# Kernel tuning notes

Measured on AMD Instinct MI355X. Metric: run time of the kernel, lower is better.

The kernel has to match this reference:

```python
import jax, jax.numpy as jnp
import numpy as np

N_ROWS = 262144
FEAT = 1024
N_CORES = 4096
SEG = N_ROWS // N_CORES
H1 = H2 = H3 = 1024
NUM_CLASSES = 2
BN_EPS = 1e-5


def setup_inputs() -> dict:
    key = jax.random.key(0)
    ks = jax.random.split(key, 12)
    x = jax.random.normal(ks[0], (N_ROWS, FEAT), dtype=jnp.float32)
    # equal-length segments: start indices 0, SEG, 2*SEG, ...
    corelen = (jnp.arange(N_CORES) * SEG).astype(jnp.int64)
    def lin(k, din, dout):
        kw, kb = jax.random.split(k)
        W = jax.random.normal(kw, (din, dout), dtype=jnp.float32) / np.sqrt(din)
        b = jnp.zeros((dout,), dtype=jnp.float32)
        return W, b
    W1, b1 = lin(ks[1], FEAT, H1)
    W2, b2 = lin(ks[2], H1, H2)
    W3, b3 = lin(ks[3], H2, H3)
    W4, b4 = lin(ks[4], H3, NUM_CLASSES)
    g1 = jnp.ones((H1,), jnp.float32); be1 = jnp.zeros((H1,), jnp.float32)
    g2 = jnp.ones((H2,), jnp.float32); be2 = jnp.zeros((H2,), jnp.float32)
    g3 = jnp.ones((H3,), jnp.float32); be3 = jnp.zeros((H3,), jnp.float32)
    return {"x": x, "corelen": corelen,
            "W1": W1, "b1": b1, "g1": g1, "be1": be1,
            "W2": W2, "b2": b2, "g2": g2, "be2": be2,
            "W3": W3, "b3": b3, "g3": g3, "be3": be3,
            "W4": W4, "b4": b4}


def _batchnorm(h, g, b):
    # BatchNorm1d, training mode: biased batch statistics over the batch dim
    m = jnp.mean(h, axis=0)
    v = jnp.mean(jnp.square(h - m), axis=0)
    return g * (h - m) * jax.lax.rsqrt(v + BN_EPS) + b


def reference(x, corelen, W1, b1, g1, be1, W2, b2, g2, be2, W3, b3, g3, be3, W4, b4):
    n = x.shape[0]
    # segment id of row r = number of starts <= r, minus 1 (rows before
    # corelen[0] get id -1 and are dropped, matching the torch loop)
    seg_ids = jnp.searchsorted(corelen, jnp.arange(n), side="right") - 1
    agg = jax.ops.segment_sum(x, seg_ids, num_segments=corelen.shape[0])  # [C, FEAT]
    h = jax.nn.relu(_batchnorm(agg @ W1 + b1, g1, be1))
    h = jax.nn.relu(_batchnorm(h @ W2 + b2, g2, be2))
    h = jax.nn.relu(_batchnorm(h @ W3 + b3, g3, be3))
    return h @ W4 + b4  # [C, NUM_CLASSES]
```

## Files before the change

kernel.cpp:

```cpp
#include <hip/hip_runtime.h>
#include <hip/hip_bf16.h>
#include <stdint.h>

#define N_ROWS 262144
#define FEAT 1024
#define N_CORES 4096
#define HDIM 1024
#define BN_EPS 1e-5f

typedef __attribute__((ext_vector_type(8))) short bf16x8;
typedef __attribute__((ext_vector_type(4))) float f32x4;

__device__ __forceinline__ unsigned short f2bf(float f) {
  __hip_bfloat16 h = __float2bfloat16(f);
  return __builtin_bit_cast(unsigned short, h);
}
__device__ __forceinline__ float bf2f(unsigned short u) {
  unsigned int x = ((unsigned int)u) << 16;
  return __builtin_bit_cast(float, x);
}

__device__ __forceinline__ void gll16(const unsigned short* g, unsigned short* l) {
  __builtin_amdgcn_global_load_lds(
      (const __attribute__((address_space(1))) void*)g,
      (__attribute__((address_space(3))) void*)l, 16, 0, 0);
}

__global__ __launch_bounds__(256)
void k_segsum(const float* __restrict__ x, const int* __restrict__ corelen,
              unsigned short* __restrict__ aggb) {
  const int seg = blockIdx.x;
  const int t = threadIdx.x;
  const int start = corelen[seg];
  const int end = (seg + 1 < N_CORES) ? corelen[seg + 1] : N_ROWS;
  float4 a0 = make_float4(0.f, 0.f, 0.f, 0.f);
  float4 a1 = make_float4(0.f, 0.f, 0.f, 0.f);
  const float* xp = x + (size_t)start * FEAT + t * 4;
  int r = start;
  for (; r + 2 <= end; r += 2) {
    const float4 v0 = *(const float4*)xp;
    const float4 v1 = *(const float4*)(xp + FEAT);
    a0.x += v0.x; a0.y += v0.y; a0.z += v0.z; a0.w += v0.w;
    a1.x += v1.x; a1.y += v1.y; a1.z += v1.z; a1.w += v1.w;
    xp += 2 * FEAT;
  }
  if (r < end) {
    const float4 v0 = *(const float4*)xp;
    a0.x += v0.x; a0.y += v0.y; a0.z += v0.z; a0.w += v0.w;
  }
  a0.x += a1.x; a0.y += a1.y; a0.z += a1.z; a0.w += a1.w;
  ushort4 o;
  o.x = f2bf(a0.x); o.y = f2bf(a0.y); o.z = f2bf(a0.z); o.w = f2bf(a0.w);
  *(ushort4*)(aggb + (size_t)seg * FEAT + t * 4) = o;
}

__global__ __launch_bounds__(256)
void k_transpose_bf16(const float* __restrict__ W, unsigned short* __restrict__ Wt) {
  __shared__ unsigned short tile[32][33];
  const int tx = threadIdx.x, ty = threadIdx.y;
  const int n0 = blockIdx.x * 32, k0 = blockIdx.y * 32;
#pragma unroll
  for (int i = 0; i < 4; ++i)
    tile[ty + 8 * i][tx] = f2bf(W[(size_t)(k0 + ty + 8 * i) * HDIM + n0 + tx]);
  __syncthreads();
#pragma unroll
  for (int i = 0; i < 4; ++i)
    Wt[(size_t)(n0 + ty + 8 * i) * HDIM + k0 + tx] = tile[tx][ty + 8 * i];
}

#define BM 128
#define BN 64
#define BK 64
__global__ __launch_bounds__(256)
void k_gemm_bt(const unsigned short* __restrict__ A,
               const unsigned short* __restrict__ Bt,
               const float* __restrict__ bias,
               float* __restrict__ C,
               float* __restrict__ sums, float* __restrict__ sumsq) {
  __shared__ unsigned short As[BM * BK];
  __shared__ unsigned short Bs[BN * BK];
  const int t = threadIdx.x;
  const int lane = t & 63;
  const int w = t >> 6;
  const int tileM = blockIdx.x * BM;
  const int tileN = blockIdx.y * BN;
  const int wr = (w >> 1) * 64;
  const int wc = (w & 1) * 32;
  const int fr = lane & 15;
  const int kk = (lane >> 4) * 8;
  const int lr = lane >> 3;
  const int sc = ((lane & 7) * 8) ^ (lr << 3);

  const unsigned short* pA = A + (size_t)(tileM + w * 32 + lr) * HDIM + sc;
  const unsigned short* pB = Bt + (size_t)(tileN + w * 16 + lr) * HDIM + sc;

  f32x4 acc[4][2] = {};

  for (int k0 = 0; k0 < HDIM; k0 += BK) {
#pragma unroll
    for (int j = 0; j < 4; ++j)
      gll16(pA + k0 + j * 8 * HDIM, As + (w * 32 + j * 8) * BK);
#pragma unroll
    for (int j = 0; j < 2; ++j)
      gll16(pB + k0 + j * 8 * HDIM, Bs + (w * 16 + j * 8) * BK);
    __syncthreads();
#pragma unroll
    for (int ks = 0; ks < 2; ++ks) {
      const int pc = (ks * 32 + kk) ^ ((fr & 7) << 3);
      bf16x8 af[4], bf[2];
#pragma unroll
      for (int m = 0; m < 4; ++m)
        af[m] = *(const bf16x8*)&As[(wr + m * 16 + fr) * BK + pc];
#pragma unroll
      for (int n = 0; n < 2; ++n)
        bf[n] = *(const bf16x8*)&Bs[(wc + n * 16 + fr) * BK + pc];
#pragma unroll
      for (int m = 0; m < 4; ++m)
#pragma unroll
        for (int n = 0; n < 2; ++n)
          acc[m][n] = __builtin_amdgcn_mfma_f32_16x16x32_bf16(af[m], bf[n], acc[m][n], 0, 0, 0);
    }
    __syncthreads();
  }

  const int cr = (lane >> 4) * 4;
  const int cc = lane & 15;
#pragma unroll
  for (int n = 0; n < 2; ++n) {
    const int col = tileN + wc + n * 16 + cc;
    const float bv = bias[col];
    float s = 0.f, s2 = 0.f;
#pragma unroll
    for (int m = 0; m < 4; ++m) {
      float* cp = C + (size_t)(tileM + wr + m * 16 + cr) * HDIM + col;
#pragma unroll
      for (int j = 0; j < 4; ++j) {
        const float h = acc[m][n][j] + bv;
        cp[(size_t)j * HDIM] = h;
        s += h; s2 += h * h;
      }
    }
    s  += __shfl_xor(s, 16, 64);  s  += __shfl_xor(s, 32, 64);
    s2 += __shfl_xor(s2, 16, 64); s2 += __shfl_xor(s2, 32, 64);
    if ((lane >> 4) == 0) {
      atomicAdd(&sums[col], s);
      atomicAdd(&sumsq[col], s2);
    }
  }
}

__global__ __launch_bounds__(256)
void k_finalize(const float* __restrict__ sums, const float* __restrict__ sumsq,
                const float* __restrict__ g, const float* __restrict__ be,
                float* __restrict__ scale, float* __restrict__ shift) {
  const int c = blockIdx.x * 256 + threadIdx.x;
  const float mean = sums[c] * (1.f / N_CORES);
  const float var = sumsq[c] * (1.f / N_CORES) - mean * mean;
  const float sc = g[c] * rsqrtf(var + BN_EPS);
  scale[c] = sc;
  shift[c] = be[c] - mean * sc;
}

__global__ __launch_bounds__(256)
void k_norm_relu(const float* __restrict__ Hp, const float* __restrict__ scale,
                 const float* __restrict__ shift, unsigned short* __restrict__ Ab) {
  const size_t i4 = ((size_t)blockIdx.x * 256 + threadIdx.x) * 4;
  const float4 v = *(const float4*)(Hp + i4);
  const int c = (int)(i4 & (HDIM - 1));
  const float4 sc = *(const float4*)(scale + c);
  const float4 sh = *(const float4*)(shift + c);
  ushort4 o;
  o.x = f2bf(fmaxf(v.x * sc.x + sh.x, 0.f));
  o.y = f2bf(fmaxf(v.y * sc.y + sh.y, 0.f));
  o.z = f2bf(fmaxf(v.z * sc.z + sh.z, 0.f));
  o.w = f2bf(fmaxf(v.w * sc.w + sh.w, 0.f));
  *(ushort4*)(Ab + i4) = o;
}

__global__ __launch_bounds__(256)
void k_final(const unsigned short* __restrict__ Ab, const float* __restrict__ W4,
             const float* __restrict__ b4, float* __restrict__ out) {
  const int t = threadIdx.x;
  const int w = t >> 6, lane = t & 63;
  const int row = blockIdx.x * 4 + w;
  const unsigned short* a = Ab + (size_t)row * HDIM + lane * 16;
  const bf16x8 v0 = *(const bf16x8*)a;
  const bf16x8 v1 = *(const bf16x8*)(a + 8);
  float s0 = 0.f, s1 = 0.f;
  const int kbase = lane * 16;
#pragma unroll
  for (int j = 0; j < 8; ++j) {
    const float av = bf2f((unsigned short)v0[j]);
    s0 += av * W4[(kbase + j) * 2 + 0];
    s1 += av * W4[(kbase + j) * 2 + 1];
  }
#pragma unroll
  for (int j = 0; j < 8; ++j) {
    const float av = bf2f((unsigned short)v1[j]);
    s0 += av * W4[(kbase + 8 + j) * 2 + 0];
    s1 += av * W4[(kbase + 8 + j) * 2 + 1];
  }
#pragma unroll
  for (int off = 32; off >= 1; off >>= 1) {
    s0 += __shfl_down(s0, off, 64);
    s1 += __shfl_down(s1, off, 64);
  }
  if (lane == 0) {
    out[row * 2 + 0] = s0 + b4[0];
    out[row * 2 + 1] = s1 + b4[1];
  }
}

extern "C" void kernel_launch(void* const* d_in, const int* in_sizes, int n_in,
                              void* d_out, int out_size, void* d_ws, size_t ws_size,
                              hipStream_t stream) {
  (void)in_sizes; (void)n_in; (void)out_size; (void)ws_size;
  const float* x       = (const float*)d_in[0];
  const int* corelen   = (const int*)d_in[1];
  const float* W1  = (const float*)d_in[2];
  const float* b1  = (const float*)d_in[3];
  const float* g1  = (const float*)d_in[4];
  const float* be1 = (const float*)d_in[5];
  const float* W2  = (const float*)d_in[6];
  const float* b2  = (const float*)d_in[7];
  const float* g2  = (const float*)d_in[8];
  const float* be2 = (const float*)d_in[9];
  const float* W3  = (const float*)d_in[10];
  const float* b3  = (const float*)d_in[11];
  const float* g3  = (const float*)d_in[12];
  const float* be3 = (const float*)d_in[13];
  const float* W4  = (const float*)d_in[14];
  const float* b4  = (const float*)d_in[15];
  float* out = (float*)d_out;

  char* ws = (char*)d_ws;
  float* Hpre          = (float*)(ws);
  unsigned short* Abf  = (unsigned short*)(ws + (16u << 20));
  unsigned short* Wt   = (unsigned short*)(ws + (24u << 20));
  float* stats = (float*)(ws + (26u << 20));
  float* scale = stats + 6 * HDIM;
  float* shift = scale + HDIM;

  hipMemsetAsync(stats, 0, 6 * HDIM * sizeof(float), stream);
  k_segsum<<<N_CORES, 256, 0, stream>>>(x, corelen, Abf);

  const float* Ws[3]  = {W1, W2, W3};
  const float* bs[3]  = {b1, b2, b3};
  const float* gs[3]  = {g1, g2, g3};
  const float* bes[3] = {be1, be2, be3};
  for (int l = 0; l < 3; ++l) {
    float* sums  = stats + l * 2 * HDIM;
    float* sumsq = sums + HDIM;
    k_transpose_bf16<<<dim3(32, 32), dim3(32, 8), 0, stream>>>(Ws[l], Wt);
    k_gemm_bt<<<dim3(N_CORES / BM, HDIM / BN), 256, 0, stream>>>(
        Abf, Wt, bs[l], Hpre, sums, sumsq);
    k_finalize<<<HDIM / 256, 256, 0, stream>>>(sums, sumsq, gs[l], bes[l], scale, shift);
    k_norm_relu<<<(N_CORES * HDIM / 4) / 256, 256, 0, stream>>>(Hpre, scale, shift, Abf);
  }
  k_final<<<N_CORES / 4, 256, 0, stream>>>(Abf, W4, b4, out);
}
```

Baseline: 300.7 us.

## Double-buffer GEMM LDS, store bf16 pre-activations, batch weight transposes

Adds double-buffered LDS staging in the GEMM so the next K tile's global-to-LDS loads are issued before computing the current one, and remaps block indices for cache locality. Pre-BatchNorm activations are stored as bf16 instead of fp32, halving traffic between GEMM and norm kernels, and the norm kernel processes 8 elements per thread. All three weight transposes run in one launch ahead of the layer loop. Storing pre-activations in bf16 adds rounding before normalization, and double buffering doubles LDS use, which may reduce occupancy.

```diff
diff --git a/kernel.cpp b/kernel.cpp
--- a/kernel.cpp
+++ b/kernel.cpp
@@ -9,6 +9,7 @@
 #define BN_EPS 1e-5f
 
 typedef __attribute__((ext_vector_type(8))) short bf16x8;
+typedef __attribute__((ext_vector_type(8))) unsigned short u16x8;
 typedef __attribute__((ext_vector_type(4))) float f32x4;
 
 __device__ __forceinline__ unsigned short f2bf(float f) {
@@ -55,8 +56,12 @@
 }
 
 __global__ __launch_bounds__(256)
-void k_transpose_bf16(const float* __restrict__ W, unsigned short* __restrict__ Wt) {
+void k_transpose_all(const float* __restrict__ W1, const float* __restrict__ W2,
+                     const float* __restrict__ W3, unsigned short* __restrict__ Wt) {
   __shared__ unsigned short tile[32][33];
+  const int l = blockIdx.z;
+  const float* W = (l == 0) ? W1 : (l == 1) ? W2 : W3;
+  unsigned short* Wo = Wt + (size_t)l * HDIM * HDIM;
   const int tx = threadIdx.x, ty = threadIdx.y;
   const int n0 = blockIdx.x * 32, k0 = blockIdx.y * 32;
 #pragma unroll
@@ -65,25 +70,28 @@
   __syncthreads();
 #pragma unroll
   for (int i = 0; i < 4; ++i)
-    Wt[(size_t)(n0 + ty + 8 * i) * HDIM + k0 + tx] = tile[tx][ty + 8 * i];
+    Wo[(size_t)(n0 + ty + 8 * i) * HDIM + k0 + tx] = tile[tx][ty + 8 * i];
 }
 
 #define BM 128
 #define BN 64
 #define BK 64
+#define NT (HDIM / BK)
 __global__ __launch_bounds__(256)
 void k_gemm_bt(const unsigned short* __restrict__ A,
                const unsigned short* __restrict__ Bt,
                const float* __restrict__ bias,
-               float* __restrict__ C,
+               unsigned short* __restrict__ C,
                float* __restrict__ sums, float* __restrict__ sumsq) {
-  __shared__ unsigned short As[BM * BK];
-  __shared__ unsigned short Bs[BN * BK];
+  __shared__ unsigned short As[2][BM * BK];
+  __shared__ unsigned short Bs[2][BN * BK];
   const int t = threadIdx.x;
   const int lane = t & 63;
   const int w = t >> 6;
-  const int tileM = blockIdx.x * BM;
-  const int tileN = blockIdx.y * BN;
+  const int bid = blockIdx.x;
+  const int rm = (bid & 7) * 64 + (bid >> 3);
+  const int tileM = (rm & 31) * BM;
+  const int tileN = (rm >> 5) * BN;
   const int wr = (w >> 1) * 64;
   const int wc = (w & 1) * 32;
   const int fr = lane & 15;
@@ -96,32 +104,38 @@
 
   f32x4 acc[4][2] = {};
 
-  for (int k0 = 0; k0 < HDIM; k0 += BK) {
-#pragma unroll
-    for (int j = 0; j < 4; ++j)
-      gll16(pA + k0 + j * 8 * HDIM, As + (w * 32 + j * 8) * BK);
-#pragma unroll
-    for (int j = 0; j < 2; ++j)
-      gll16(pB + k0 + j * 8 * HDIM, Bs + (w * 16 + j * 8) * BK);
-    __syncthreads();
+#define STAGE(buf, k0)                                                   \
+  {                                                                      \
+    _Pragma("unroll") for (int j = 0; j < 4; ++j)                        \
+        gll16(pA + (k0) + j * 8 * HDIM, &As[buf][(w * 32 + j * 8) * BK]);\
+    _Pragma("unroll") for (int j = 0; j < 2; ++j)                        \
+        gll16(pB + (k0) + j * 8 * HDIM, &Bs[buf][(w * 16 + j * 8) * BK]);\
+  }
+
+  STAGE(0, 0);
+  __syncthreads();
+  for (int kt = 0; kt < NT; ++kt) {
+    const int cur = kt & 1;
+    if (kt < NT - 1) STAGE(cur ^ 1, (kt + 1) * BK);
 #pragma unroll
     for (int ks = 0; ks < 2; ++ks) {
       const int pc = (ks * 32 + kk) ^ ((fr & 7) << 3);
-      bf16x8 af[4], bf[2];
+      bf16x8 af[4], bfv[2];
 #pragma unroll
       for (int m = 0; m < 4; ++m)
-        af[m] = *(const bf16x8*)&As[(wr + m * 16 + fr) * BK + pc];
+        af[m] = *(const bf16x8*)&As[cur][(wr + m * 16 + fr) * BK + pc];
 #pragma unroll
       for (int n = 0; n < 2; ++n)
-        bf[n] = *(const bf16x8*)&Bs[(wc + n * 16 + fr) * BK + pc];
+        bfv[n] = *(const bf16x8*)&Bs[cur][(wc + n * 16 + fr) * BK + pc];
 #pragma unroll
       for (int m = 0; m < 4; ++m)
 #pragma unroll
         for (int n = 0; n < 2; ++n)
-          acc[m][n] = __builtin_amdgcn_mfma_f32_16x16x32_bf16(af[m], bf[n], acc[m][n], 0, 0, 0);
+          acc[m][n] = __builtin_amdgcn_mfma_f32_16x16x32_bf16(af[m], bfv[n], acc[m][n], 0, 0, 0);
     }
     __syncthreads();
   }
+#undef STAGE
 
   const int cr = (lane >> 4) * 4;
   const int cc = lane & 15;
@@ -132,11 +146,11 @@
     float s = 0.f, s2 = 0.f;
 #pragma unroll
     for (int m = 0; m < 4; ++m) {
-      float* cp = C + (size_t)(tileM + wr + m * 16 + cr) * HDIM + col;
+      unsigned short* cp = C + (size_t)(tileM + wr + m * 16 + cr) * HDIM + col;
 #pragma unroll
       for (int j = 0; j < 4; ++j) {
         const float h = acc[m][n][j] + bv;
-        cp[(size_t)j * HDIM] = h;
+        cp[(size_t)j * HDIM] = f2bf(h);
         s += h; s2 += h * h;
       }
     }
@@ -162,19 +176,25 @@
 }
 
 __global__ __launch_bounds__(256)
-void k_norm_relu(const float* __restrict__ Hp, const float* __restrict__ scale,
+void k_norm_relu(const unsigned short* __restrict__ Hb, const float* __restrict__ scale,
                  const float* __restrict__ shift, unsigned short* __restrict__ Ab) {
-  const size_t i4 = ((size_t)blockIdx.x * 256 + threadIdx.x) * 4;
-  const float4 v = *(const float4*)(Hp + i4);
-  const int c = (int)(i4 & (HDIM - 1));
-  const float4 sc = *(const float4*)(scale + c);
-  const float4 sh = *(const float4*)(shift + c);
-  ushort4 o;
-  o.x = f2bf(fmaxf(v.x * sc.x + sh.x, 0.f));
-  o.y = f2bf(fmaxf(v.y * sc.y + sh.y, 0.f));
-  o.z = f2bf(fmaxf(v.z * sc.z + sh.z, 0.f));
-  o.w = f2bf(fmaxf(v.w * sc.w + sh.w, 0.f));
-  *(ushort4*)(Ab + i4) = o;
+  const size_t i8 = ((size_t)blockIdx.x * 256 + threadIdx.x) * 8;
+  const u16x8 v = *(const u16x8*)(Hb + i8);
+  const int c = (int)(i8 & (HDIM - 1));
+  const float4 sc0 = *(const float4*)(scale + c);
+  const float4 sc1 = *(const float4*)(scale + c + 4);
+  const float4 sh0 = *(const float4*)(shift + c);
+  const float4 sh1 = *(const float4*)(shift + c + 4);
+  u16x8 o;
+  o[0] = f2bf(fmaxf(bf2f(v[0]) * sc0.x + sh0.x, 0.f));
+  o[1] = f2bf(fmaxf(bf2f(v[1]) * sc0.y + sh0.y, 0.f));
+  o[2] = f2bf(fmaxf(bf2f(v[2]) * sc0.z + sh0.z, 0.f));
+  o[3] = f2bf(fmaxf(bf2f(v[3]) * sc0.w + sh0.w, 0.f));
+  o[4] = f2bf(fmaxf(bf2f(v[4]) * sc1.x + sh1.x, 0.f));
+  o[5] = f2bf(fmaxf(bf2f(v[5]) * sc1.y + sh1.y, 0.f));
+  o[6] = f2bf(fmaxf(bf2f(v[6]) * sc1.z + sh1.z, 0.f));
+  o[7] = f2bf(fmaxf(bf2f(v[7]) * sc1.w + sh1.w, 0.f));
+  *(u16x8*)(Ab + i8) = o;
 }
 
 __global__ __launch_bounds__(256)
@@ -234,28 +254,27 @@
   float* out = (float*)d_out;
 
   char* ws = (char*)d_ws;
-  float* Hpre          = (float*)(ws);
-  unsigned short* Abf  = (unsigned short*)(ws + (16u << 20));
-  unsigned short* Wt   = (unsigned short*)(ws + (24u << 20));
-  float* stats = (float*)(ws + (26u << 20));
+  unsigned short* Hb   = (unsigned short*)(ws);
+  unsigned short* Abf  = (unsigned short*)(ws + (8u << 20));
+  unsigned short* Wt   = (unsigned short*)(ws + (16u << 20));
+  float* stats = (float*)(ws + (22u << 20));
   float* scale = stats + 6 * HDIM;
   float* shift = scale + HDIM;
 
   hipMemsetAsync(stats, 0, 6 * HDIM * sizeof(float), stream);
+  k_transpose_all<<<dim3(32, 32, 3), dim3(32, 8), 0, stream>>>(W1, W2, W3, Wt);
   k_segsum<<<N_CORES, 256, 0, stream>>>(x, corelen, Abf);
 
-  const float* Ws[3]  = {W1, W2, W3};
   const float* bs[3]  = {b1, b2, b3};
   const float* gs[3]  = {g1, g2, g3};
   const float* bes[3] = {be1, be2, be3};
   for (int l = 0; l < 3; ++l) {
     float* sums  = stats + l * 2 * HDIM;
     float* sumsq = sums + HDIM;
-    k_transpose_bf16<<<dim3(32, 32), dim3(32, 8), 0, stream>>>(Ws[l], Wt);
-    k_gemm_bt<<<dim3(N_CORES / BM, HDIM / BN), 256, 0, stream>>>(
-        Abf, Wt, bs[l], Hpre, sums, sumsq);
+    k_gemm_bt<<<(N_CORES / BM) * (HDIM / BN), 256, 0, stream>>>(
+        Abf, Wt + (size_t)l * HDIM * HDIM, bs[l], Hb, sums, sumsq);
     k_finalize<<<HDIM / 256, 256, 0, stream>>>(sums, sumsq, gs[l], bes[l], scale, shift);
-    k_norm_relu<<<(N_CORES * HDIM / 4) / 256, 256, 0, stream>>>(Hpre, scale, shift, Abf);
+    k_norm_relu<<<(N_CORES * HDIM / 8) / 256, 256, 0, stream>>>(Hb, scale, shift, Abf);
   }
   k_final<<<N_CORES / 4, 256, 0, stream>>>(Abf, W4, b4, out);
 }
```

Result: slower. 322.8 us (+7.4%).
